# Performance work log

Hardware: AMD Instinct MI355X
Metric: run time of the kernel (lower is better)

Reference implementation:

```python
import jax, jax.numpy as jnp
import numpy as np

N_NODES = 50000
N_EDGES = 800000
IN_FEATS = 512
OUT_FEATS = 512
DROP_P = 0.1


def setup_inputs() -> dict:
    key = jax.random.key(0)
    k1, k2, k3, k4, k5 = jax.random.split(key, 5)
    x = jax.random.normal(k1, (N_NODES, IN_FEATS), dtype=jnp.float32)
    edge_w = jax.random.uniform(k2, (N_EDGES,), dtype=jnp.float32)
    W = jax.random.normal(k3, (IN_FEATS, OUT_FEATS), dtype=jnp.float32) * (1.0 / np.sqrt(IN_FEATS))
    b = jnp.zeros((OUT_FEATS,), dtype=jnp.float32)
    edge_src = jax.random.randint(k4, (N_EDGES,), 0, N_NODES, dtype=jnp.int32)
    edge_dst = jnp.sort(jax.random.randint(k5, (N_EDGES,), 0, N_NODES, dtype=jnp.int32))
    return {"x": x, "edge_w": edge_w, "W": W, "b": b,
            "edge_src": edge_src, "edge_dst": edge_dst}


def reference(x, edge_w, W, b, edge_src, edge_dst):
    # Dropout (train mode, p=0.1) with a fixed key for determinism.
    keep = jax.random.bernoulli(jax.random.key(42), 1.0 - DROP_P, x.shape)
    xd = jnp.where(keep, x / (1.0 - DROP_P), 0.0)
    # Sparse adjacency matmul: out[dst] += adj_w * x[src]  (torch.spmm(adj, x))
    msgs = xd[edge_src] * edge_w[:, None]          # [E, in_feats]
    agg = jax.ops.segment_sum(msgs, edge_dst, num_segments=N_NODES)  # [N, in_feats]
    # Linear + ReLU activation
    return jax.nn.relu(agg @ W + b)
```

## Files before the change

kernel.cpp:

```cpp
#include <hip/hip_runtime.h>
#include <hip/hip_bf16.h>
#include <stdint.h>


#define N_NODESC 50000
#define N_EDGESC 800000
#define FEATS    512
#define TOT_ELEMS (N_NODESC * FEATS)

#define DROP_BLKS   12500
#define WCONV_BLKS  1024
#define ROWP_BLKS   3126
#define PREP_BLKS   (DROP_BLKS + WCONV_BLKS + ROWP_BLKS)

typedef unsigned int u32;
typedef unsigned short u16;
typedef __attribute__((ext_vector_type(8))) short short8;
typedef __attribute__((ext_vector_type(4))) float floatx4;

__device__ __forceinline__ void tf_round(u32& a, u32& b, int r) {
  a += b;
  b = (b << r) | (b >> (32 - r));
  b ^= a;
}

__device__ __forceinline__ void threefry(u32& x0, u32& x1) {
  const u32 k0 = 0u, k1 = 42u, k2 = 0x1BD11BDAu ^ 0u ^ 42u;
  x0 += k0; x1 += k1;
  tf_round(x0,x1,13); tf_round(x0,x1,15); tf_round(x0,x1,26); tf_round(x0,x1,6);
  x0 += k1; x1 += k2 + 1u;
  tf_round(x0,x1,17); tf_round(x0,x1,29); tf_round(x0,x1,16); tf_round(x0,x1,24);
  x0 += k2; x1 += k0 + 2u;
  tf_round(x0,x1,13); tf_round(x0,x1,15); tf_round(x0,x1,26); tf_round(x0,x1,6);
  x0 += k0; x1 += k1 + 3u;
  tf_round(x0,x1,17); tf_round(x0,x1,29); tf_round(x0,x1,16); tf_round(x0,x1,24);
  x0 += k1; x1 += k2 + 4u;
  tf_round(x0,x1,13); tf_round(x0,x1,15); tf_round(x0,x1,26); tf_round(x0,x1,6);
  x0 += k2; x1 += k0 + 5u;
}

__device__ __forceinline__ u16 f2bf(float f) {
  u32 u = __float_as_uint(f);
  u32 r = (u + 0x7FFFu + ((u >> 16) & 1u)) >> 16;
  return (u16)r;
}

__global__ __launch_bounds__(256) void prep_kernel(const float* __restrict__ x,
                                                   u16* __restrict__ xd,
                                                   const float* __restrict__ W,
                                                   u16* __restrict__ WbT,
                                                   const int* __restrict__ dst,
                                                   int* __restrict__ rowptr) {
  int b = blockIdx.x;
  if (b < DROP_BLKS) {
    int t = b * 256 + threadIdx.x;
    int j0 = t * 8;
    float4 xa = *(const float4*)(x + j0);
    float4 xb = *(const float4*)(x + j0 + 4);
    float xs[8] = {xa.x, xa.y, xa.z, xa.w, xb.x, xb.y, xb.z, xb.w};
    u16 r[8];
#pragma unroll
    for (int q = 0; q < 8; ++q) {
      u32 a = 0u, c = (u32)(j0 + q);
      threefry(a, c);
      u32 bits = a ^ c;
      float u = __uint_as_float((bits >> 9) | 0x3F800000u) - 1.0f;
      float m = (u < 0.9f) ? (1.0f / 0.9f) : 0.0f;
      r[q] = f2bf(xs[q] * m);
    }
    uint4 o;
    o.x = (u32)r[0] | ((u32)r[1] << 16);
    o.y = (u32)r[2] | ((u32)r[3] << 16);
    o.z = (u32)r[4] | ((u32)r[5] << 16);
    o.w = (u32)r[6] | ((u32)r[7] << 16);
    *(uint4*)(xd + j0) = o;
  } else if (b < DROP_BLKS + WCONV_BLKS) {
    int t = (b - DROP_BLKS) * 256 + threadIdx.x;
    int k = t >> 9, n = t & 511;
    WbT[n * 512 + k] = f2bf(W[t]);
  } else {
    int e = (b - DROP_BLKS - WCONV_BLKS) * 256 + threadIdx.x;
    if (e > N_EDGESC) return;
    int d  = (e < N_EDGESC) ? dst[e] : N_NODESC;
    int pd = (e > 0) ? dst[e - 1] : -1;
    for (int n = pd + 1; n <= d; ++n) rowptr[n] = e;
  }
}

__device__ __forceinline__ void agg_fma(float* acc, float w, const uint4& v) {
  u32 a[4] = {v.x, v.y, v.z, v.w};
#pragma unroll
  for (int p = 0; p < 4; ++p) {
    acc[2*p]   += w * __uint_as_float(a[p] << 16);
    acc[2*p+1] += w * __uint_as_float(a[p] & 0xFFFF0000u);
  }
}

__global__ __launch_bounds__(256) void agg_kernel(const u16* __restrict__ xd,
                                                  const float* __restrict__ ew,
                                                  const int* __restrict__ src,
                                                  const int* __restrict__ rowptr,
                                                  u16* __restrict__ agg) {
  int node = blockIdx.x * 4 + (threadIdx.x >> 6);
  if (node >= N_NODESC) return;
  int lane = threadIdx.x & 63;
  int lo = rowptr[node];
  int hi = rowptr[node + 1];
  float acc[8] = {0.f,0.f,0.f,0.f,0.f,0.f,0.f,0.f};

  int e = lo;
  for (; e + 8 <= hi; e += 8) {
    uint4 v[8]; float w[8];
#pragma unroll
    for (int q = 0; q < 8; ++q) {
      int s = src[e + q];
      w[q] = ew[e + q];
      v[q] = ((const uint4*)(xd + (size_t)s * FEATS))[lane];
    }
#pragma unroll
    for (int q = 0; q < 8; ++q) agg_fma(acc, w[q], v[q]);
  }
  if (e + 4 <= hi) {
    uint4 v[4]; float w[4];
#pragma unroll
    for (int q = 0; q < 4; ++q) {
      int s = src[e + q];
      w[q] = ew[e + q];
      v[q] = ((const uint4*)(xd + (size_t)s * FEATS))[lane];
    }
#pragma unroll
    for (int q = 0; q < 4; ++q) agg_fma(acc, w[q], v[q]);
    e += 4;
  }
  for (; e < hi; ++e) {
    float w = ew[e];
    int s = src[e];
    uint4 v = ((const uint4*)(xd + (size_t)s * FEATS))[lane];
    agg_fma(acc, w, v);
  }

  uint4 o;
  o.x = (u32)f2bf(acc[0]) | ((u32)f2bf(acc[1]) << 16);
  o.y = (u32)f2bf(acc[2]) | ((u32)f2bf(acc[3]) << 16);
  o.z = (u32)f2bf(acc[4]) | ((u32)f2bf(acc[5]) << 16);
  o.w = (u32)f2bf(acc[6]) | ((u32)f2bf(acc[7]) << 16);
  ((uint4*)(agg + (size_t)node * FEATS))[lane] = o;
}

#define BM 128
#define BN 256
#define BK 64

__global__ __launch_bounds__(512, 4) void gemm_kernel(const u16* __restrict__ A,
                                                      const u16* __restrict__ BT,
                                                      const float* __restrict__ bias,
                                                      float* __restrict__ out) {
  __shared__ __align__(16) u16 Asm[BM * BK];
  __shared__ __align__(16) u16 Bsm[BN * BK];

  const int tid  = threadIdx.x;
  const int lane = tid & 63;
  const int w    = tid >> 6;
  const int m0 = blockIdx.x * BM;
  const int n0 = blockIdx.y * BN;
  const int wm = (w >> 2) * 64;
  const int wn = (w & 3) * 64;
  const int lm   = lane & 15;
  const int quad = lane >> 4;
  const int lrow = lane >> 3;
  const int lcol = (lane & 7) * 8;

  floatx4 acc[4][4];
#pragma unroll
  for (int i = 0; i < 4; ++i)
#pragma unroll
    for (int j = 0; j < 4; ++j) acc[i][j] = (floatx4)0.0f;

  for (int k0 = 0; k0 < 512; k0 += BK) {
#pragma unroll
    for (int t = 0; t < 2; ++t) {
      int chunk = w * 2 + t;
      int row = chunk * 8 + lrow;
      int gm = m0 + row;
      if (gm > N_NODESC - 1) gm = N_NODESC - 1;
      __builtin_amdgcn_global_load_lds(
          (const __attribute__((address_space(1))) void*)(A + (size_t)gm * 512 + k0 + lcol),
          (__attribute__((address_space(3))) void*)((char*)Asm + chunk * 1024),
          16, 0, 0);
    }
#pragma unroll
    for (int t = 0; t < 4; ++t) {
      int chunk = w * 4 + t;
      int row = chunk * 8 + lrow;
      __builtin_amdgcn_global_load_lds(
          (const __attribute__((address_space(1))) void*)(BT + (size_t)(n0 + row) * 512 + k0 + lcol),
          (__attribute__((address_space(3))) void*)((char*)Bsm + chunk * 1024),
          16, 0, 0);
    }
    __syncthreads();

#pragma unroll
    for (int kk = 0; kk < BK; kk += 32) {
      short8 af[4], bfr[4];
#pragma unroll
      for (int i = 0; i < 4; ++i)
        af[i] = *(const short8*)(Asm + (wm + i * 16 + lm) * BK + kk + quad * 8);
#pragma unroll
      for (int j = 0; j < 4; ++j)
        bfr[j] = *(const short8*)(Bsm + (wn + j * 16 + lm) * BK + kk + quad * 8);
#pragma unroll
      for (int i = 0; i < 4; ++i)
#pragma unroll
        for (int j = 0; j < 4; ++j)
          acc[i][j] = __builtin_amdgcn_mfma_f32_16x16x32_bf16(af[i], bfr[j], acc[i][j], 0, 0, 0);
    }
    __syncthreads();
  }

#pragma unroll
  for (int j = 0; j < 4; ++j) {
    int col = n0 + wn + j * 16 + lm;
    float bv = bias[col];
#pragma unroll
    for (int i = 0; i < 4; ++i) {
      int row0 = m0 + wm + i * 16 + quad * 4;
#pragma unroll
      for (int r = 0; r < 4; ++r) {
        int row = row0 + r;
        if (row < N_NODESC) {
          float v = acc[i][j][r] + bv;
          out[(size_t)row * 512 + col] = v > 0.0f ? v : 0.0f;
        }
      }
    }
  }
}

extern "C" void kernel_launch(void* const* d_in, const int* in_sizes, int n_in,
                              void* d_out, int out_size, void* d_ws, size_t ws_size,
                              hipStream_t stream) {
  const float* x  = (const float*)d_in[0];
  const float* ew = (const float*)d_in[1];
  const float* W  = (const float*)d_in[2];
  const float* b  = (const float*)d_in[3];
  const int* esrc = (const int*)d_in[4];
  const int* edst = (const int*)d_in[5];
  float* out = (float*)d_out;

  char* ws = (char*)d_ws;
  u16* xd    = (u16*)ws;
  u16* agg   = (u16*)(ws + (size_t)TOT_ELEMS * 2);
  u16* WbT   = (u16*)(ws + (size_t)TOT_ELEMS * 4);
  int* rowp  = (int*)(ws + (size_t)TOT_ELEMS * 4 + 512 * 512 * 2);
  (void)ws_size; (void)n_in; (void)in_sizes; (void)out_size;

  hipLaunchKernelGGL(prep_kernel,  dim3(PREP_BLKS), dim3(256), 0, stream,
                     x, xd, W, WbT, edst, rowp);
  hipLaunchKernelGGL(agg_kernel,   dim3((N_NODESC + 3) / 4), dim3(256), 0, stream,
                     xd, ew, esrc, rowp, agg);
  hipLaunchKernelGGL(gemm_kernel,  dim3((N_NODESC + BM - 1) / BM, 512 / BN), dim3(512), 0, stream,
                     agg, WbT, b, out);
}
```

Baseline: 363.5 us.

## Store dropout output in feature-sliced planes and aggregate per slice for cache locality

```diff
diff --git a/kernel.cpp b/kernel.cpp
--- a/kernel.cpp
+++ b/kernel.cpp
@@ -8,15 +8,21 @@
 #define FEATS    512
 #define TOT_ELEMS (N_NODESC * FEATS)
 
+#define PLANE_STRIDE (N_NODESC * 32)
+
 #define DROP_BLKS   12500
 #define WCONV_BLKS  1024
 #define ROWP_BLKS   3126
 #define PREP_BLKS   (DROP_BLKS + WCONV_BLKS + ROWP_BLKS)
 
+#define AGG_NG      782
+#define AGG_BLKS    (AGG_NG * 8)
+
 typedef unsigned int u32;
 typedef unsigned short u16;
 typedef __attribute__((ext_vector_type(8))) short short8;
 typedef __attribute__((ext_vector_type(4))) float floatx4;
+typedef __attribute__((ext_vector_type(4))) u32 uintx4;
 
 __device__ __forceinline__ void tf_round(u32& a, u32& b, int r) {
   a += b;
@@ -73,7 +79,9 @@
     o.y = (u32)r[2] | ((u32)r[3] << 16);
     o.z = (u32)r[4] | ((u32)r[5] << 16);
     o.w = (u32)r[6] | ((u32)r[7] << 16);
-    *(uint4*)(xd + j0) = o;
+    int node = j0 >> 9;
+    int f0 = j0 & 511;
+    *(uint4*)(xd + (size_t)(f0 >> 5) * PLANE_STRIDE + node * 32 + (f0 & 31)) = o;
   } else if (b < DROP_BLKS + WCONV_BLKS) {
     int t = (b - DROP_BLKS) * 256 + threadIdx.x;
     int k = t >> 9, n = t & 511;
@@ -100,51 +108,49 @@
                                                   const float* __restrict__ ew,
                                                   const int* __restrict__ src,
                                                   const int* __restrict__ rowptr,
-                                                  u16* __restrict__ agg) {
-  int node = blockIdx.x * 4 + (threadIdx.x >> 6);
-  if (node >= N_NODESC) return;
-  int lane = threadIdx.x & 63;
-  int lo = rowptr[node];
-  int hi = rowptr[node + 1];
+                                                  u16* __restrict__ agg,
+                                                  int phase) {
+  const int s8    = blockIdx.x & 7;
+  const int g     = blockIdx.x >> 3;
+  const int slice = s8 + phase * 8;
+  const int wv    = threadIdx.x >> 6;
+  const int lane  = threadIdx.x & 63;
+  const int grp   = lane >> 2;
+  const int fl    = lane & 3;
+
+  const int n = g * 64 + wv * 16 + grp;
+  int lo = 0, hi = 0;
+  if (n < N_NODESC) { lo = rowptr[n]; hi = rowptr[n + 1]; }
+
+  const u16* plane = xd + (size_t)slice * PLANE_STRIDE;
   float acc[8] = {0.f,0.f,0.f,0.f,0.f,0.f,0.f,0.f};
 
-  int e = lo;
-  for (; e + 8 <= hi; e += 8) {
+  for (int e0 = lo; __any(e0 < hi); e0 += 8) {
     uint4 v[8]; float w[8];
 #pragma unroll
     for (int q = 0; q < 8; ++q) {
-      int s = src[e + q];
-      w[q] = ew[e + q];
-      v[q] = ((const uint4*)(xd + (size_t)s * FEATS))[lane];
+      int e = e0 + q;
+      v[q] = (uint4){0u,0u,0u,0u};
+      w[q] = 0.0f;
+      if (e < hi) {
+        int s = __builtin_nontemporal_load(src + e);
+        w[q] = __builtin_nontemporal_load(ew + e);
+        v[q] = *(const uint4*)(plane + (size_t)s * 32 + fl * 8);
+      }
     }
 #pragma unroll
     for (int q = 0; q < 8; ++q) agg_fma(acc, w[q], v[q]);
   }
-  if (e + 4 <= hi) {
-    uint4 v[4]; float w[4];
-#pragma unroll
-    for (int q = 0; q < 4; ++q) {
-      int s = src[e + q];
-      w[q] = ew[e + q];
-      v[q] = ((const uint4*)(xd + (size_t)s * FEATS))[lane];
-    }
-#pragma unroll
-    for (int q = 0; q < 4; ++q) agg_fma(acc, w[q], v[q]);
-    e += 4;
-  }
-  for (; e < hi; ++e) {
-    float w = ew[e];
-    int s = src[e];
-    uint4 v = ((const uint4*)(xd + (size_t)s * FEATS))[lane];
-    agg_fma(acc, w, v);
-  }
-
-  uint4 o;
-  o.x = (u32)f2bf(acc[0]) | ((u32)f2bf(acc[1]) << 16);
-  o.y = (u32)f2bf(acc[2]) | ((u32)f2bf(acc[3]) << 16);
-  o.z = (u32)f2bf(acc[4]) | ((u32)f2bf(acc[5]) << 16);
-  o.w = (u32)f2bf(acc[6]) | ((u32)f2bf(acc[7]) << 16);
-  ((uint4*)(agg + (size_t)node * FEATS))[lane] = o;
+
+  if (n < N_NODESC) {
+    uintx4 o;
+    o.x = (u32)f2bf(acc[0]) | ((u32)f2bf(acc[1]) << 16);
+    o.y = (u32)f2bf(acc[2]) | ((u32)f2bf(acc[3]) << 16);
+    o.z = (u32)f2bf(acc[4]) | ((u32)f2bf(acc[5]) << 16);
+    o.w = (u32)f2bf(acc[6]) | ((u32)f2bf(acc[7]) << 16);
+    __builtin_nontemporal_store(o,
+        (uintx4*)(agg + (size_t)n * 512 + slice * 32 + fl * 8));
+  }
 }
 
 #define BM 128
@@ -256,8 +262,10 @@
 
   hipLaunchKernelGGL(prep_kernel,  dim3(PREP_BLKS), dim3(256), 0, stream,
                      x, xd, W, WbT, edst, rowp);
-  hipLaunchKernelGGL(agg_kernel,   dim3((N_NODESC + 3) / 4), dim3(256), 0, stream,
-                     xd, ew, esrc, rowp, agg);
+  hipLaunchKernelGGL(agg_kernel,   dim3(AGG_BLKS), dim3(256), 0, stream,
+                     xd, ew, esrc, rowp, agg, 0);
+  hipLaunchKernelGGL(agg_kernel,   dim3(AGG_BLKS), dim3(256), 0, stream,
+                     xd, ew, esrc, rowp, agg, 1);
   hipLaunchKernelGGL(gemm_kernel,  dim3((N_NODESC + BM - 1) / BM, 512 / BN), dim3(512), 0, stream,
                      agg, WbT, b, out);
 }
```

Measured after the change: 600.2 us. 65.1% more time.

## Fuse sparse aggregation and dense GEMM into one kernel via LDS tile

Applied to the files above, without the earlier changes.

```diff
diff --git a/kernel.cpp b/kernel.cpp
--- a/kernel.cpp
+++ b/kernel.cpp
@@ -12,6 +12,9 @@
 #define WCONV_BLKS  1024
 #define ROWP_BLKS   3126
 #define PREP_BLKS   (DROP_BLKS + WCONV_BLKS + ROWP_BLKS)
+
+#define BMF 64
+#define FUSE_BLKS ((N_NODESC + BMF - 1) / BMF)
 
 typedef unsigned int u32;
 typedef unsigned short u16;
@@ -96,79 +99,70 @@
   }
 }
 
-__global__ __launch_bounds__(256) void agg_kernel(const u16* __restrict__ xd,
-                                                  const float* __restrict__ ew,
-                                                  const int* __restrict__ src,
-                                                  const int* __restrict__ rowptr,
-                                                  u16* __restrict__ agg) {
-  int node = blockIdx.x * 4 + (threadIdx.x >> 6);
-  if (node >= N_NODESC) return;
-  int lane = threadIdx.x & 63;
-  int lo = rowptr[node];
-  int hi = rowptr[node + 1];
-  float acc[8] = {0.f,0.f,0.f,0.f,0.f,0.f,0.f,0.f};
-
-  int e = lo;
-  for (; e + 8 <= hi; e += 8) {
-    uint4 v[8]; float w[8];
-#pragma unroll
-    for (int q = 0; q < 8; ++q) {
-      int s = src[e + q];
-      w[q] = ew[e + q];
-      v[q] = ((const uint4*)(xd + (size_t)s * FEATS))[lane];
-    }
-#pragma unroll
-    for (int q = 0; q < 8; ++q) agg_fma(acc, w[q], v[q]);
-  }
-  if (e + 4 <= hi) {
-    uint4 v[4]; float w[4];
-#pragma unroll
-    for (int q = 0; q < 4; ++q) {
-      int s = src[e + q];
-      w[q] = ew[e + q];
-      v[q] = ((const uint4*)(xd + (size_t)s * FEATS))[lane];
-    }
-#pragma unroll
-    for (int q = 0; q < 4; ++q) agg_fma(acc, w[q], v[q]);
-    e += 4;
-  }
-  for (; e < hi; ++e) {
-    float w = ew[e];
-    int s = src[e];
-    uint4 v = ((const uint4*)(xd + (size_t)s * FEATS))[lane];
-    agg_fma(acc, w, v);
-  }
-
-  uint4 o;
-  o.x = (u32)f2bf(acc[0]) | ((u32)f2bf(acc[1]) << 16);
-  o.y = (u32)f2bf(acc[2]) | ((u32)f2bf(acc[3]) << 16);
-  o.z = (u32)f2bf(acc[4]) | ((u32)f2bf(acc[5]) << 16);
-  o.w = (u32)f2bf(acc[6]) | ((u32)f2bf(acc[7]) << 16);
-  ((uint4*)(agg + (size_t)node * FEATS))[lane] = o;
-}
-
-#define BM 128
-#define BN 256
-#define BK 64
-
-__global__ __launch_bounds__(512, 4) void gemm_kernel(const u16* __restrict__ A,
-                                                      const u16* __restrict__ BT,
-                                                      const float* __restrict__ bias,
-                                                      float* __restrict__ out) {
-  __shared__ __align__(16) u16 Asm[BM * BK];
-  __shared__ __align__(16) u16 Bsm[BN * BK];
-
-  const int tid  = threadIdx.x;
-  const int lane = tid & 63;
-  const int w    = tid >> 6;
-  const int m0 = blockIdx.x * BM;
-  const int n0 = blockIdx.y * BN;
-  const int wm = (w >> 2) * 64;
-  const int wn = (w & 3) * 64;
+__global__ __launch_bounds__(512, 4) void fused_kernel(const u16* __restrict__ xd,
+                                                       const float* __restrict__ ew,
+                                                       const int* __restrict__ src,
+                                                       const int* __restrict__ rowptr,
+                                                       const u16* __restrict__ WbT,
+                                                       const float* __restrict__ bias,
+                                                       float* __restrict__ out) {
+  __shared__ __align__(16) u16 Atile[BMF * 512];
+
+  const int w    = threadIdx.x >> 6;
+  const int lane = threadIdx.x & 63;
+  const int m0   = blockIdx.x * BMF;
+
+#pragma unroll 1
+  for (int i = 0; i < 8; ++i) {
+    const int r    = w * 8 + i;
+    const int node = m0 + r;
+    float acc[8] = {0.f,0.f,0.f,0.f,0.f,0.f,0.f,0.f};
+    if (node < N_NODESC) {
+      int lo = rowptr[node];
+      int hi = rowptr[node + 1];
+      int e = lo;
+      for (; e + 8 <= hi; e += 8) {
+        uint4 v[8]; float wt[8];
+#pragma unroll
+        for (int q = 0; q < 8; ++q) {
+          int s = src[e + q];
+          wt[q] = ew[e + q];
+          v[q] = ((const uint4*)(xd + (size_t)s * FEATS))[lane];
+        }
+#pragma unroll
+        for (int q = 0; q < 8; ++q) agg_fma(acc, wt[q], v[q]);
+      }
+      if (e + 4 <= hi) {
+        uint4 v[4]; float wt[4];
+#pragma unroll
+        for (int q = 0; q < 4; ++q) {
+          int s = src[e + q];
+          wt[q] = ew[e + q];
+          v[q] = ((const uint4*)(xd + (size_t)s * FEATS))[lane];
+        }
+#pragma unroll
+        for (int q = 0; q < 4; ++q) agg_fma(acc, wt[q], v[q]);
+        e += 4;
+      }
+      for (; e < hi; ++e) {
+        float wt = ew[e];
+        int s = src[e];
+        uint4 v = ((const uint4*)(xd + (size_t)s * FEATS))[lane];
+        agg_fma(acc, wt, v);
+      }
+    }
+    uint4 o;
+    o.x = (u32)f2bf(acc[0]) | ((u32)f2bf(acc[1]) << 16);
+    o.y = (u32)f2bf(acc[2]) | ((u32)f2bf(acc[3]) << 16);
+    o.z = (u32)f2bf(acc[4]) | ((u32)f2bf(acc[5]) << 16);
+    o.w = (u32)f2bf(acc[6]) | ((u32)f2bf(acc[7]) << 16);
+    *(uint4*)((char*)Atile + r * 1024 + ((lane * 16) ^ ((r & 7) << 4))) = o;
+  }
+  __syncthreads();
+
+  const int wn   = w * 64;
   const int lm   = lane & 15;
   const int quad = lane >> 4;
-  const int lrow = lane >> 3;
-  const int lcol = (lane & 7) * 8;
 
   floatx4 acc[4][4];
 #pragma unroll
@@ -176,54 +170,34 @@
 #pragma unroll
     for (int j = 0; j < 4; ++j) acc[i][j] = (floatx4)0.0f;
 
-  for (int k0 = 0; k0 < 512; k0 += BK) {
-#pragma unroll
-    for (int t = 0; t < 2; ++t) {
-      int chunk = w * 2 + t;
-      int row = chunk * 8 + lrow;
-      int gm = m0 + row;
-      if (gm > N_NODESC - 1) gm = N_NODESC - 1;
-      __builtin_amdgcn_global_load_lds(
-          (const __attribute__((address_space(1))) void*)(A + (size_t)gm * 512 + k0 + lcol),
-          (__attribute__((address_space(3))) void*)((char*)Asm + chunk * 1024),
-          16, 0, 0);
-    }
-#pragma unroll
-    for (int t = 0; t < 4; ++t) {
-      int chunk = w * 4 + t;
-      int row = chunk * 8 + lrow;
-      __builtin_amdgcn_global_load_lds(
-          (const __attribute__((address_space(1))) void*)(BT + (size_t)(n0 + row) * 512 + k0 + lcol),
-          (__attribute__((address_space(3))) void*)((char*)Bsm + chunk * 1024),
-          16, 0, 0);
-    }
-    __syncthreads();
-
-#pragma unroll
-    for (int kk = 0; kk < BK; kk += 32) {
-      short8 af[4], bfr[4];
-#pragma unroll
-      for (int i = 0; i < 4; ++i)
-        af[i] = *(const short8*)(Asm + (wm + i * 16 + lm) * BK + kk + quad * 8);
+#pragma unroll 4
+  for (int k0 = 0; k0 < 512; k0 += 32) {
+    short8 af[4], bfr[4];
+#pragma unroll
+    for (int i = 0; i < 4; ++i) {
+      int r = i * 16 + lm;
+      af[i] = *(const short8*)((const char*)Atile + r * 1024 +
+                               ((u32)(k0 * 2 + quad * 16) ^ ((r & 7) << 4)));
+    }
+#pragma unroll
+    for (int j = 0; j < 4; ++j) {
+      int n = wn + j * 16 + lm;
+      bfr[j] = *(const short8*)(WbT + (size_t)n * 512 + k0 + quad * 8);
+    }
+#pragma unroll
+    for (int i = 0; i < 4; ++i)
 #pragma unroll
       for (int j = 0; j < 4; ++j)
-        bfr[j] = *(const short8*)(Bsm + (wn + j * 16 + lm) * BK + kk + quad * 8);
-#pragma unroll
-      for (int i = 0; i < 4; ++i)
-#pragma unroll
-        for (int j = 0; j < 4; ++j)
-          acc[i][j] = __builtin_amdgcn_mfma_f32_16x16x32_bf16(af[i], bfr[j], acc[i][j], 0, 0, 0);
-    }
-    __syncthreads();
+        acc[i][j] = __builtin_amdgcn_mfma_f32_16x16x32_bf16(af[i], bfr[j], acc[i][j], 0, 0, 0);
   }
 
 #pragma unroll
   for (int j = 0; j < 4; ++j) {
-    int col = n0 + wn + j * 16 + lm;
+    int col = wn + j * 16 + lm;
     float bv = bias[col];
 #pragma unroll
     for (int i = 0; i < 4; ++i) {
-      int row0 = m0 + wm + i * 16 + quad * 4;
+      int row0 = m0 + i * 16 + quad * 4;
 #pragma unroll
       for (int r = 0; r < 4; ++r) {
         int row = row0 + r;
@@ -249,15 +223,12 @@
 
   char* ws = (char*)d_ws;
   u16* xd    = (u16*)ws;
-  u16* agg   = (u16*)(ws + (size_t)TOT_ELEMS * 2);
-  u16* WbT   = (u16*)(ws + (size_t)TOT_ELEMS * 4);
-  int* rowp  = (int*)(ws + (size_t)TOT_ELEMS * 4 + 512 * 512 * 2);
+  u16* WbT   = (u16*)(ws + (size_t)TOT_ELEMS * 2);
+  int* rowp  = (int*)(ws + (size_t)TOT_ELEMS * 2 + 512 * 512 * 2);
   (void)ws_size; (void)n_in; (void)in_sizes; (void)out_size;
 
   hipLaunchKernelGGL(prep_kernel,  dim3(PREP_BLKS), dim3(256), 0, stream,
                      x, xd, W, WbT, edst, rowp);
-  hipLaunchKernelGGL(agg_kernel,   dim3((N_NODESC + 3) / 4), dim3(256), 0, stream,
-                     xd, ew, esrc, rowp, agg);
-  hipLaunchKernelGGL(gemm_kernel,  dim3((N_NODESC + BM - 1) / BM, 512 / BN), dim3(512), 0, stream,
-                     agg, WbT, b, out);
-}
+  hipLaunchKernelGGL(fused_kernel, dim3(FUSE_BLKS), dim3(512), 0, stream,
+                     xd, ew, esrc, rowp, WbT, b, out);
+}
```

New measurement: 395.2 us. 1.09x slower.

## Double-buffer GEMM shared-memory tiles with BK=32 to overlap loads and MFMA

Applied to the files above, without the earlier changes.

```diff
diff --git a/kernel.cpp b/kernel.cpp
--- a/kernel.cpp
+++ b/kernel.cpp
@@ -149,14 +149,14 @@
 
 #define BM 128
 #define BN 256
-#define BK 64
+#define BK 32
 
 __global__ __launch_bounds__(512, 4) void gemm_kernel(const u16* __restrict__ A,
                                                       const u16* __restrict__ BT,
                                                       const float* __restrict__ bias,
                                                       float* __restrict__ out) {
-  __shared__ __align__(16) u16 Asm[BM * BK];
-  __shared__ __align__(16) u16 Bsm[BN * BK];
+  __shared__ __align__(16) u16 Asm[2][BM * BK];
+  __shared__ __align__(16) u16 Bsm[2][BN * BK];
 
   const int tid  = threadIdx.x;
   const int lane = tid & 63;
@@ -167,8 +167,30 @@
   const int wn = (w & 3) * 64;
   const int lm   = lane & 15;
   const int quad = lane >> 4;
-  const int lrow = lane >> 3;
-  const int lcol = (lane & 7) * 8;
+  const int srow = lane >> 2;
+  const int scol = (lane & 3) * 8;
+
+  int a_gm = m0 + w * 16 + srow;
+  if (a_gm > N_NODESC - 1) a_gm = N_NODESC - 1;
+  const u16* a_src = A + (size_t)a_gm * 512 + scol;
+  const u16* b_src0 = BT + (size_t)(n0 + w * 32 + srow) * 512 + scol;
+  const u16* b_src1 = BT + (size_t)(n0 + w * 32 + 16 + srow) * 512 + scol;
+
+#define STAGE(buf, k0)                                                        \
+  do {                                                                        \
+    __builtin_amdgcn_global_load_lds(                                         \
+        (const __attribute__((address_space(1))) void*)(a_src + (k0)),        \
+        (__attribute__((address_space(3))) void*)((char*)Asm[buf] + w * 1024 + lane * 16), \
+        16, 0, 0);                                                            \
+    __builtin_amdgcn_global_load_lds(                                         \
+        (const __attribute__((address_space(1))) void*)(b_src0 + (k0)),       \
+        (__attribute__((address_space(3))) void*)((char*)Bsm[buf] + (w * 2) * 1024 + lane * 16), \
+        16, 0, 0);                                                            \
+    __builtin_amdgcn_global_load_lds(                                         \
+        (const __attribute__((address_space(1))) void*)(b_src1 + (k0)),       \
+        (__attribute__((address_space(3))) void*)((char*)Bsm[buf] + (w * 2 + 1) * 1024 + lane * 16), \
+        16, 0, 0);                                                            \
+  } while (0)
 
   floatx4 acc[4][4];
 #pragma unroll
@@ -176,46 +198,30 @@
 #pragma unroll
     for (int j = 0; j < 4; ++j) acc[i][j] = (floatx4)0.0f;
 
-  for (int k0 = 0; k0 < 512; k0 += BK) {
-#pragma unroll
-    for (int t = 0; t < 2; ++t) {
-      int chunk = w * 2 + t;
-      int row = chunk * 8 + lrow;
-      int gm = m0 + row;
-      if (gm > N_NODESC - 1) gm = N_NODESC - 1;
-      __builtin_amdgcn_global_load_lds(
-          (const __attribute__((address_space(1))) void*)(A + (size_t)gm * 512 + k0 + lcol),
-          (__attribute__((address_space(3))) void*)((char*)Asm + chunk * 1024),
-          16, 0, 0);
-    }
-#pragma unroll
-    for (int t = 0; t < 4; ++t) {
-      int chunk = w * 4 + t;
-      int row = chunk * 8 + lrow;
-      __builtin_amdgcn_global_load_lds(
-          (const __attribute__((address_space(1))) void*)(BT + (size_t)(n0 + row) * 512 + k0 + lcol),
-          (__attribute__((address_space(3))) void*)((char*)Bsm + chunk * 1024),
-          16, 0, 0);
-    }
+  STAGE(0, 0);
+  __syncthreads();
+
+#pragma unroll 1
+  for (int t = 0; t < 512 / BK; ++t) {
+    const int cur = t & 1;
+    if (t < 512 / BK - 1) STAGE(cur ^ 1, (t + 1) * BK);
+
+    short8 af[4], bfr[4];
+#pragma unroll
+    for (int i = 0; i < 4; ++i)
+      af[i] = *(const short8*)(Asm[cur] + (wm + i * 16 + lm) * BK + quad * 8);
+#pragma unroll
+    for (int j = 0; j < 4; ++j)
+      bfr[j] = *(const short8*)(Bsm[cur] + (wn + j * 16 + lm) * BK + quad * 8);
+#pragma unroll
+    for (int i = 0; i < 4; ++i)
+#pragma unroll
+      for (int j = 0; j < 4; ++j)
+        acc[i][j] = __builtin_amdgcn_mfma_f32_16x16x32_bf16(af[i], bfr[j], acc[i][j], 0, 0, 0);
+
     __syncthreads();
-
-#pragma unroll
-    for (int kk = 0; kk < BK; kk += 32) {
-      short8 af[4], bfr[4];
-#pragma unroll
-      for (int i = 0; i < 4; ++i)
-        af[i] = *(const short8*)(Asm + (wm + i * 16 + lm) * BK + kk + quad * 8);
-#pragma unroll
-      for (int j = 0; j < 4; ++j)
-        bfr[j] = *(const short8*)(Bsm + (wn + j * 16 + lm) * BK + kk + quad * 8);
-#pragma unroll
-      for (int i = 0; i < 4; ++i)
-#pragma unroll
-        for (int j = 0; j < 4; ++j)
-          acc[i][j] = __builtin_amdgcn_mfma_f32_16x16x32_bf16(af[i], bfr[j], acc[i][j], 0, 0, 0);
-    }
-    __syncthreads();
-  }
+  }
+#undef STAGE
 
 #pragma unroll
   for (int j = 0; j < 4; ++j) {
```

Result: no change. 359.0 us, median of 2 (-1.2%).
